# Optimization experiments

Measured on AMD Instinct MI355X. Metric: run time of the kernel, lower is better.

Reference implementation:

```python
import jax, jax.numpy as jnp
import numpy as np

ALPHA = 0.2          # LeakyReLU negative slope
NEG_INF = -9e15      # mask value used by the original module


def setup_inputs() -> dict:
    key = jax.random.key(0)
    k1, k2, k3, k4 = jax.random.split(key, 4)
    N, F_IN, F_OUT = 8192, 512, 256
    inp = jax.random.normal(k1, (N, F_IN), dtype=jnp.float32)
    W = jax.random.normal(k2, (F_IN, F_OUT), dtype=jnp.float32) * (1.414 / np.sqrt(F_IN))
    a = jax.random.normal(k3, (2 * F_OUT, 1), dtype=jnp.float32) * (1.414 / np.sqrt(F_OUT))
    adj = jax.random.randint(k4, (N, N), 0, 2, dtype=jnp.int32)
    return {"input": inp, "W": W, "a": a, "adj": adj}


def reference(input, W, a, adj):
    # h: [N, F_out]
    h = input @ W
    F_out = h.shape[1]
    # Original builds a_input[i,j] = concat(h_i, h_j) then matmuls with a.
    # Equivalent: e_ij = leakyrelu(h_i . a[:F] + h_j . a[F:]) without the O(N^2 * 2F) tensor.
    a1 = a[:F_out, 0]   # [F_out]
    a2 = a[F_out:, 0]   # [F_out]
    s1 = h @ a1         # [N]
    s2 = h @ a2         # [N]
    e = jax.nn.leaky_relu(s1[:, None] + s2[None, :], negative_slope=ALPHA)  # [N, N]
    attention = jax.nn.softmax(jnp.where(adj > 0, e, NEG_INF), axis=1)       # [N, N]
    return attention @ h  # [N, F_out]
```

## Files before the change

### kernel.cpp

```cpp
#include <hip/hip_runtime.h>


typedef __attribute__((ext_vector_type(8))) short bf16x8;
typedef __attribute__((ext_vector_type(4))) float fx4;
typedef __attribute__((ext_vector_type(4))) int ix4;
typedef __attribute__((ext_vector_type(2))) unsigned int ux2;

#define NN 8192
#define FIN 512
#define FOUT 256
#define PS 136
#define AROWS 32

__device__ __forceinline__ unsigned short f2bf(float f) {
    unsigned int x = __float_as_uint(f);
    x += 0x7fffu + ((x >> 16) & 1u);
    return (unsigned short)(x >> 16);
}
__device__ __forceinline__ bf16x8 pack8(fx4 a, fx4 b) {
    bf16x8 r;
    r[0] = (short)f2bf(a[0]); r[1] = (short)f2bf(a[1]);
    r[2] = (short)f2bf(a[2]); r[3] = (short)f2bf(a[3]);
    r[4] = (short)f2bf(b[0]); r[5] = (short)f2bf(b[1]);
    r[6] = (short)f2bf(b[2]); r[7] = (short)f2bf(b[3]);
    return r;
}

__global__ void wt_kernel(const float* __restrict__ W,
                          unsigned short* __restrict__ WTt) {
    const int c = threadIdx.x;
    const int k = blockIdx.x;
    WTt[((size_t)(k >> 5) * 256 + c) * 32 + (k & 31)] = f2bf(W[k * FOUT + c]);
}

__global__ __launch_bounds__(256) void prep_kernel(
    const float* __restrict__ X,
    const unsigned short* __restrict__ WTt,
    const float* __restrict__ A,
    const int* __restrict__ adj,
    unsigned short* __restrict__ hTt,
    float* __restrict__ s1, float* __restrict__ s2,
    unsigned int* __restrict__ mask)
{
    __shared__ float s1sh[4][16], s2sh[4][16];
    const int tid = threadIdx.x;

    if (blockIdx.x >= 512) {
        const int g = (blockIdx.x - 512) * 256 + tid;
        const int* base = adj + (size_t)g * 32;
        ix4 v[8];
#pragma unroll
        for (int k = 0; k < 8; ++k) v[k] = *(const ix4*)(base + k * 4);
        unsigned int m = 0;
#pragma unroll
        for (int k = 0; k < 8; ++k)
#pragma unroll
            for (int j = 0; j < 4; ++j)
                m |= (v[k][j] != 0 ? 1u : 0u) << (k * 4 + j);
        mask[g] = m;
        return;
    }

    const int w = tid >> 6, l = tid & 63, q = l >> 4, lr = l & 15;
    const int r0 = blockIdx.x * 16;
    const int cbase = w * 64;
    fx4 acc[4] = {};

    for (int kb = 0; kb < FIN; kb += 32) {
        const float* xp = X + (size_t)(r0 + lr) * FIN + kb + q * 8;
        bf16x8 a0 = pack8(*(const fx4*)xp, *(const fx4*)(xp + 4));
#pragma unroll
        for (int tc = 0; tc < 4; ++tc) {
            bf16x8 b = *(const bf16x8*)(WTt + ((size_t)(kb >> 5) * 256 + cbase + tc * 16 + lr) * 32 + q * 8);
            acc[tc] = __builtin_amdgcn_mfma_f32_16x16x32_bf16(a0, b, acc[tc], 0, 0, 0);
        }
    }

    const int jb = r0 >> 5, jo = (r0 & 31) + q * 4;
#pragma unroll
    for (int tc = 0; tc < 4; ++tc) {
        const int c = cbase + tc * 16 + lr;
        ux2 hp;
        hp.x = (unsigned)f2bf(acc[tc][0]) | ((unsigned)f2bf(acc[tc][1]) << 16);
        hp.y = (unsigned)f2bf(acc[tc][2]) | ((unsigned)f2bf(acc[tc][3]) << 16);
        *(ux2*)(hTt + ((size_t)jb * 256 + c) * 32 + jo) = hp;
    }

    float p1[4] = {}, p2[4] = {};
#pragma unroll
    for (int tc = 0; tc < 4; ++tc) {
        const int c = cbase + tc * 16 + lr;
        const float a1v = A[c], a2v = A[FOUT + c];
#pragma unroll
        for (int r = 0; r < 4; ++r) {
            p1[r] += acc[tc][r] * a1v;
            p2[r] += acc[tc][r] * a2v;
        }
    }
#pragma unroll
    for (int r = 0; r < 4; ++r) {
#pragma unroll
        for (int off = 1; off < 16; off <<= 1) {
            p1[r] += __shfl_xor(p1[r], off);
            p2[r] += __shfl_xor(p2[r], off);
        }
        if (lr == 0) { s1sh[w][q * 4 + r] = p1[r]; s2sh[w][q * 4 + r] = p2[r]; }
    }
    __syncthreads();
    if (tid < 16) {
        s1[r0 + tid] = s1sh[0][tid] + s1sh[1][tid] + s1sh[2][tid] + s1sh[3][tid];
        s2[r0 + tid] = s2sh[0][tid] + s2sh[1][tid] + s2sh[2][tid] + s2sh[3][tid];
    }
}

__global__ __launch_bounds__(512) void attn_kernel(
    const unsigned int* __restrict__ mask,
    const unsigned short* __restrict__ hTt,
    const float* __restrict__ s1,
    const float* __restrict__ s2,
    float* __restrict__ out)
{
    __shared__ unsigned short P[2][AROWS * PS];
    __shared__ float dsh[AROWS];

    const int tid = threadIdx.x;
    const int r0 = blockIdx.x * AROWS;

    const int prow = tid >> 4;
    const int pq = tid & 15;
    const float s1v = s1[r0 + prow];
    const unsigned int* mrow = mask + (size_t)(r0 + prow) * 256;
    const int mshift = (pq & 3) * 8;
    float denp = 0.f;

    const int w = tid >> 6, l = tid & 63, q = l >> 4, lr = l & 15;
    const int cbase = w * 32;
    fx4 acc[2][2] = {};

    struct LSet { unsigned int mval; fx4 s2a, s2b; };
    LSet LA, LB;
    bf16x8 B0[4][2], B1[4][2];

    auto loadP = [&](int kt, LSet& L) {
        L.mval = mrow[kt * 4 + (pq >> 2)];
        L.s2a = *(const fx4*)(s2 + kt * 128 + pq * 8);
        L.s2b = *(const fx4*)(s2 + kt * 128 + pq * 8 + 4);
    };
    auto calcP = [&](int b, const LSet& L) {
        const unsigned int mbyte = (L.mval >> mshift) & 0xFFu;
        bf16x8 pv;
#pragma unroll
        for (int j = 0; j < 8; ++j) {
            const float s2j = (j < 4) ? L.s2a[j] : L.s2b[j - 4];
            float t = s1v + s2j;
            float e = fmaxf(t, 0.2f * t);
            e = fminf(e, 30.f);
            const float p = ((mbyte >> j) & 1u) ? __expf(e) : 0.f;
            denp += p;
            pv[j] = (short)f2bf(p);
        }
        *(bf16x8*)(&P[b][prow * PS + pq * 8]) = pv;
    };
    auto loadB = [&](int it, bf16x8 (&B)[4][2]) {
#pragma unroll
        for (int ks = 0; ks < 4; ++ks)
#pragma unroll
            for (int tc = 0; tc < 2; ++tc)
                B[ks][tc] = *(const bf16x8*)(hTt + ((size_t)(it * 4 + ks) * 256 + cbase + tc * 16 + lr) * 32 + q * 8);
    };

    const int ITERS = NN / 128;
    loadP(0, LA);
    calcP(0, LA);
    loadP(1, LA);
    loadB(0, B0);
    __syncthreads();

    auto body = [&](int it, bf16x8 (&Bc)[4][2], bf16x8 (&Bn)[4][2],
                    LSet& Lc, LSet& Ln) {
        if (it + 1 < ITERS) loadB(it + 1, Bn);
        if (it + 2 < ITERS) loadP(it + 2, Ln);
        const unsigned short* Pb = P[it & 1];
        bf16x8 af0[4], af1[4];
#pragma unroll
        for (int ks = 0; ks < 4; ++ks) {
            af0[ks] = *(const bf16x8*)(Pb + lr * PS + ks * 32 + q * 8);
            af1[ks] = *(const bf16x8*)(Pb + (16 + lr) * PS + ks * 32 + q * 8);
        }
#pragma unroll
        for (int ks = 0; ks < 4; ++ks)
#pragma unroll
            for (int tc = 0; tc < 2; ++tc) {
                acc[0][tc] = __builtin_amdgcn_mfma_f32_16x16x32_bf16(af0[ks], Bc[ks][tc], acc[0][tc], 0, 0, 0);
                acc[1][tc] = __builtin_amdgcn_mfma_f32_16x16x32_bf16(af1[ks], Bc[ks][tc], acc[1][tc], 0, 0, 0);
            }
        if (it + 1 < ITERS) calcP((it + 1) & 1, Lc);
        __syncthreads();
    };

    for (int it = 0; it < ITERS; it += 2) {
        body(it, B0, B1, LA, LB);
        body(it + 1, B1, B0, LB, LA);
    }

    float v = denp;
    v += __shfl_xor(v, 1);
    v += __shfl_xor(v, 2);
    v += __shfl_xor(v, 4);
    v += __shfl_xor(v, 8);
    if (pq == 0) dsh[prow] = v;
    __syncthreads();

#pragma unroll
    for (int mg = 0; mg < 2; ++mg) {
#pragma unroll
        for (int r = 0; r < 4; ++r) {
            const int row = mg * 16 + q * 4 + r;
            const float dinv = 1.0f / fmaxf(dsh[row], 1e-30f);
#pragma unroll
            for (int tc = 0; tc < 2; ++tc) {
                out[(size_t)(r0 + row) * FOUT + cbase + tc * 16 + lr] = acc[mg][tc][r] * dinv;
            }
        }
    }
}

extern "C" void kernel_launch(void* const* d_in, const int* in_sizes, int n_in,
                              void* d_out, int out_size, void* d_ws, size_t ws_size,
                              hipStream_t stream) {
    const float *X = nullptr, *W = nullptr, *A = nullptr;
    const int* adj = nullptr;
    for (int i = 0; i < n_in; ++i) {
        switch (in_sizes[i]) {
            case NN * FIN:   X = (const float*)d_in[i]; break;
            case FIN * FOUT: W = (const float*)d_in[i]; break;
            case 2 * FOUT:   A = (const float*)d_in[i]; break;
            case NN * NN:    adj = (const int*)d_in[i]; break;
        }
    }
    if (!X) X = (const float*)d_in[0];
    if (!W) W = (const float*)d_in[1];
    if (!A) A = (const float*)d_in[2];
    if (!adj) adj = (const int*)d_in[3];
    float* out = (float*)d_out;

    char* ws = (char*)d_ws;
    float* s1 = (float*)ws;
    float* s2 = (float*)(ws + 32768);
    unsigned short* WTt = (unsigned short*)(ws + 98304);
    unsigned short* hTt = (unsigned short*)(ws + 360448);
    unsigned int* mask = (unsigned int*)(ws + 5242880);

    wt_kernel<<<512, 256, 0, stream>>>(W, WTt);
    prep_kernel<<<512 + 8192, 256, 0, stream>>>(X, WTt, A, adj, hTt, s1, s2, mask);
    attn_kernel<<<NN / AROWS, 512, 0, stream>>>(mask, hTt, s1, s2, out);
}
```

Baseline: 467.3 us.

## Split attention tile into 64 rows by 128 output columns per block

```diff
diff --git a/kernel.cpp b/kernel.cpp
--- a/kernel.cpp
+++ b/kernel.cpp
@@ -10,7 +10,7 @@
 #define FIN 512
 #define FOUT 256
 #define PS 136
-#define AROWS 32
+#define AROWS 64
 
 __device__ __forceinline__ unsigned short f2bf(float f) {
     unsigned int x = __float_as_uint(f);
@@ -124,42 +124,50 @@
     __shared__ float dsh[AROWS];
 
     const int tid = threadIdx.x;
-    const int r0 = blockIdx.x * AROWS;
-
-    const int prow = tid >> 4;
-    const int pq = tid & 15;
+    const int rg = blockIdx.x >> 1;
+    const int ch = blockIdx.x & 1;
+    const int r0 = rg * AROWS;
+    const int c0 = ch * 128;
+
+    const int prow = tid >> 3;
+    const int pq8 = tid & 7;
     const float s1v = s1[r0 + prow];
     const unsigned int* mrow = mask + (size_t)(r0 + prow) * 256;
-    const int mshift = (pq & 3) * 8;
+    const int mdw = pq8 >> 1;
+    const int mshift = (pq8 & 1) * 16;
     float denp = 0.f;
 
     const int w = tid >> 6, l = tid & 63, q = l >> 4, lr = l & 15;
-    const int cbase = w * 32;
+    const int wr = (w >> 2) * 32;
+    const int cbase = c0 + (w & 3) * 32;
     fx4 acc[2][2] = {};
 
-    struct LSet { unsigned int mval; fx4 s2a, s2b; };
+    struct LSet { unsigned int mval; fx4 s2v[4]; };
     LSet LA, LB;
     bf16x8 B0[4][2], B1[4][2];
 
     auto loadP = [&](int kt, LSet& L) {
-        L.mval = mrow[kt * 4 + (pq >> 2)];
-        L.s2a = *(const fx4*)(s2 + kt * 128 + pq * 8);
-        L.s2b = *(const fx4*)(s2 + kt * 128 + pq * 8 + 4);
+        L.mval = mrow[kt * 4 + mdw];
+        const float* s2p = s2 + kt * 128 + pq8 * 16;
+#pragma unroll
+        for (int j = 0; j < 4; ++j) L.s2v[j] = *(const fx4*)(s2p + j * 4);
     };
     auto calcP = [&](int b, const LSet& L) {
-        const unsigned int mbyte = (L.mval >> mshift) & 0xFFu;
-        bf16x8 pv;
-#pragma unroll
-        for (int j = 0; j < 8; ++j) {
-            const float s2j = (j < 4) ? L.s2a[j] : L.s2b[j - 4];
-            float t = s1v + s2j;
+        const unsigned int m16 = (L.mval >> mshift) & 0xFFFFu;
+        bf16x8 pv0, pv1;
+#pragma unroll
+        for (int j = 0; j < 16; ++j) {
+            const float t = s1v + L.s2v[j >> 2][j & 3];
             float e = fmaxf(t, 0.2f * t);
             e = fminf(e, 30.f);
-            const float p = ((mbyte >> j) & 1u) ? __expf(e) : 0.f;
+            const float p = ((m16 >> j) & 1u) ? __expf(e) : 0.f;
             denp += p;
-            pv[j] = (short)f2bf(p);
-        }
-        *(bf16x8*)(&P[b][prow * PS + pq * 8]) = pv;
+            if (j < 8) pv0[j] = (short)f2bf(p);
+            else       pv1[j - 8] = (short)f2bf(p);
+        }
+        unsigned short* dst = &P[b][prow * PS + pq8 * 16];
+        *(bf16x8*)dst = pv0;
+        *(bf16x8*)(dst + 8) = pv1;
     };
     auto loadB = [&](int it, bf16x8 (&B)[4][2]) {
 #pragma unroll
@@ -184,8 +192,8 @@
         bf16x8 af0[4], af1[4];
 #pragma unroll
         for (int ks = 0; ks < 4; ++ks) {
-            af0[ks] = *(const bf16x8*)(Pb + lr * PS + ks * 32 + q * 8);
-            af1[ks] = *(const bf16x8*)(Pb + (16 + lr) * PS + ks * 32 + q * 8);
+            af0[ks] = *(const bf16x8*)(Pb + (wr + lr) * PS + ks * 32 + q * 8);
+            af1[ks] = *(const bf16x8*)(Pb + (wr + 16 + lr) * PS + ks * 32 + q * 8);
         }
 #pragma unroll
         for (int ks = 0; ks < 4; ++ks)
@@ -207,15 +215,14 @@
     v += __shfl_xor(v, 1);
     v += __shfl_xor(v, 2);
     v += __shfl_xor(v, 4);
-    v += __shfl_xor(v, 8);
-    if (pq == 0) dsh[prow] = v;
+    if (pq8 == 0) dsh[prow] = v;
     __syncthreads();
 
 #pragma unroll
     for (int mg = 0; mg < 2; ++mg) {
 #pragma unroll
         for (int r = 0; r < 4; ++r) {
-            const int row = mg * 16 + q * 4 + r;
+            const int row = wr + mg * 16 + q * 4 + r;
             const float dinv = 1.0f / fmaxf(dsh[row], 1e-30f);
 #pragma unroll
             for (int tc = 0; tc < 2; ++tc) {
@@ -253,5 +260,5 @@
 
     wt_kernel<<<512, 256, 0, stream>>>(W, WTt);
     prep_kernel<<<512 + 8192, 256, 0, stream>>>(X, WTt, A, adj, hTt, s1, s2, mask);
-    attn_kernel<<<NN / AROWS, 512, 0, stream>>>(mask, hTt, s1, s2, out);
-}
+    attn_kernel<<<(NN / AROWS) * 2, 512, 0, stream>>>(mask, hTt, s1, s2, out);
+}
```

Result: slower. 503.9 us (+7.8%).
